# Performance work log

Measured on AMD Instinct MI355X. Metric: run time of the kernel, lower is better.

The kernel has to match this reference:

```python
import jax, jax.numpy as jnp
import numpy as np

B, T, F, H, C = 256, 14, 1024, 1024, 2513


def lstm_step(Wih, Whh, bih, bhh, x, h, c):
    # PyTorch LSTM cell: gate order i, f, g, o
    g = x @ Wih.T + bih + h @ Whh.T + bhh
    i, f, gg, o = jnp.split(g, 4, axis=-1)
    i = jax.nn.sigmoid(i)
    f = jax.nn.sigmoid(f)
    gg = jnp.tanh(gg)
    o = jax.nn.sigmoid(o)
    c = f * c + i * gg
    h = o * jnp.tanh(c)
    return h, c


def setup_inputs() -> dict:
    key = jax.random.key(0)
    ks = jax.random.split(key, 11)
    s = 1.0 / np.sqrt(H)
    u = lambda k, shape: jax.random.uniform(k, shape, jnp.float32, -s, s)
    return {
        "inputs": jax.random.normal(ks[0], (B, T, F), jnp.float32),
        "roll_Wih": u(ks[1], (4 * H, F)),
        "roll_Whh": u(ks[2], (4 * H, H)),
        "roll_bih": u(ks[3], (4 * H,)),
        "roll_bhh": u(ks[4], (4 * H,)),
        "unroll_Wih": u(ks[5], (4 * H, F)),
        "unroll_Whh": u(ks[6], (4 * H, H)),
        "unroll_bih": u(ks[7], (4 * H,)),
        "unroll_bhh": u(ks[8], (4 * H,)),
        "cls_W": u(ks[9], (C, H)),
        "cls_b": u(ks[10], (C,)),
    }


def reference(inputs, roll_Wih, roll_Whh, roll_bih, roll_bhh,
              unroll_Wih, unroll_Whh, unroll_bih, unroll_bhh, cls_W, cls_b):
    x_t = jnp.transpose(inputs, (1, 0, 2))  # [T, B, F]

    # Rolling LSTM: scan over time, keep hidden/cell at every step
    h0 = jnp.zeros((B, H), inputs.dtype)
    c0 = jnp.zeros((B, H), inputs.dtype)

    def roll(carry, xt):
        h, c = carry
        h, c = lstm_step(roll_Wih, roll_Whh, roll_bih, roll_bhh, xt, h, c)
        return (h, c), (h, c)

    _, (hs, cs) = jax.lax.scan(roll, (h0, c0), x_t)  # each [T, B, H]

    # Unrolling LSTM: for each t, feed inputs[t] repeated (T - t + 1) times,
    # starting from (hs[t], cs[t]). Vectorized over t: run T+1 steps for all
    # branches with constant per-branch input x_t[t], then pick step (T - t).
    def unroll(carry, _):
        h, c = carry  # [T, B, H]
        h, c = lstm_step(unroll_Wih, unroll_Whh, unroll_bih, unroll_bhh, x_t, h, c)
        return (h, c), h

    _, h_all = jax.lax.scan(unroll, (hs, cs), None, length=T + 1)  # [T+1, T, B, H]
    t_idx = jnp.arange(T)
    h_n = h_all[T - t_idx, t_idx]  # [T, B, H], last output of each branch

    x = jnp.transpose(h_n, (1, 0, 2))  # [B, T, H]
    y = x @ cls_W.T + cls_b  # [B, T, C]
    return y
```

## Files before the change

### kernel.cpp

```cpp
#include <hip/hip_runtime.h>

#define DEVFN __device__ __forceinline__

typedef __bf16 bf16x8 __attribute__((ext_vector_type(8)));
typedef float floatx4 __attribute__((ext_vector_type(4)));
typedef unsigned short us4 __attribute__((ext_vector_type(4)));


DEVFN unsigned short f2bf(float x) {
    union { float f; unsigned u; } v; v.f = x;
    v.u += 0x7FFFu + ((v.u >> 16) & 1u);
    return (unsigned short)(v.u >> 16);
}

DEVFN float bf2f(unsigned short s) {
    union { unsigned u; float f; } v; v.u = ((unsigned)s) << 16; return v.f;
}

DEVFN float sigm(float x) { return 1.f / (1.f + __expf(-x)); }
DEVFN float tanh_fast(float x) { float t = __expf(2.f * x); return 1.f - 2.f / (t + 1.f); }

DEVFN void gload_lds16(const unsigned short* g, unsigned short* l) {
    __builtin_amdgcn_global_load_lds(
        (__attribute__((address_space(1))) unsigned int*)g,
        (__attribute__((address_space(3))) unsigned int*)l, 16, 0, 0);
}

#define CFENCE asm volatile("" ::: "memory")


__global__ __launch_bounds__(256) void transpose_bt(const float* __restrict__ in,
                                                    unsigned short* __restrict__ out) {
    int idx = blockIdx.x * 256 + threadIdx.x;
    int k4 = (idx & 255) << 2;
    int row = idx >> 8;
    int t = row >> 8, b = row & 255;
    float4 v = *(const float4*)(in + (size_t)(b * 14 + t) * 1024 + k4);
    us4 o = {f2bf(v.x), f2bf(v.y), f2bf(v.z), f2bf(v.w)};
    *(us4*)(out + (size_t)row * 1024 + k4) = o;
}

__global__ __launch_bounds__(256) void conv_w4(const float* __restrict__ s0, const float* __restrict__ s1,
                                               const float* __restrict__ s2, const float* __restrict__ s3,
                                               unsigned short* __restrict__ d0, unsigned short* __restrict__ d1,
                                               unsigned short* __restrict__ d2, unsigned short* __restrict__ d3) {
    int t = blockIdx.x * 256 + threadIdx.x;
    int which = t >> 20;
    int off = (t & 1048575) << 2;
    const float* s = (which == 0) ? s0 : (which == 1) ? s1 : (which == 2) ? s2 : s3;
    unsigned short* d = (which == 0) ? d0 : (which == 1) ? d1 : (which == 2) ? d2 : d3;
    float4 v = *(const float4*)(s + off);
    us4 o = {f2bf(v.x), f2bf(v.y), f2bf(v.z), f2bf(v.w)};
    *(us4*)(d + off) = o;
}

__global__ __launch_bounds__(256) void conv_cls(const float* __restrict__ in,
                                                unsigned short* __restrict__ out) {
    int t = blockIdx.x * 256 + threadIdx.x;
    int off = t << 2;
    us4 o = {0, 0, 0, 0};
    if (off < 2573312) {
        float4 v = *(const float4*)(in + off);
        o = (us4){f2bf(v.x), f2bf(v.y), f2bf(v.z), f2bf(v.w)};
    }
    *(us4*)(out + off) = o;
}

__global__ __launch_bounds__(256) void bias_interleave(const float* __restrict__ a,
                                                       const float* __restrict__ b,
                                                       float* __restrict__ o4, int n) {
    int i = blockIdx.x * 256 + threadIdx.x;
    if (i < n) {
        int g = i >> 10, h = i & 1023;
        o4[h * 4 + g] = a[i] + b[i];
    }
}

__global__ __launch_bounds__(256) void cell_only(const unsigned short* __restrict__ pre4b,
                                                 float* __restrict__ c_out,
                                                 unsigned short* __restrict__ h_out) {
    int idx = blockIdx.x * 256 + threadIdx.x;
    us4 pv = *(const us4*)(pre4b + (size_t)idx * 4);
    float iv = sigm(bf2f(pv.x)), fv = sigm(bf2f(pv.y));
    float gv = tanh_fast(bf2f(pv.z)), ov = sigm(bf2f(pv.w));
    float cn = iv * gv;
    float hn = ov * tanh_fast(cn);
    c_out[idx] = cn;
    h_out[idx] = f2bf(hn);
}

template <int MODE, int NH>
__global__ __launch_bounds__(256, 2)
void lstm_big(const unsigned short* __restrict__ A1, const unsigned short* __restrict__ W1,
              const unsigned short* __restrict__ pre4b,
              const float* __restrict__ bias4,
              const float* __restrict__ c_in,
              float* __restrict__ c_out,
              unsigned short* __restrict__ h_out,
              unsigned short* __restrict__ h_alt, int retire_t,
              unsigned short* __restrict__ gout_bf,
              const float* __restrict__ clsb,
              float* __restrict__ outp, int gx) {
    constexpr int BROWS = 4 * NH;
    constexpr int FN = BROWS / 32;
    constexpr int BISS = BROWS / 64;
    constexpr int LOADS = 2 + BISS;
    constexpr int ASH = 4096;
    constexpr int BSH = BROWS * 32;
    constexpr int HH = NH / 32;

    __shared__ __align__(16) unsigned short lds[2][ASH + BSH];

    const int tid = threadIdx.x;
    const int nwg = gridDim.x;
    int id = blockIdx.x;
    id = ((id & 7) * (nwg >> 3)) + (id >> 3);
    const int bx = id % gx;
    const int by = id / gx;
    const int m0 = by * 128;
    const int n0h = bx * NH;
    const int n0c = bx * BROWS;
    const int lane = tid & 63;
    const int wv = tid >> 6;
    const int wm = wv >> 1, wn = wv & 1;
    const int r16 = lane & 15;
    const int kg = lane >> 4;

    auto stage = [&](int u, int buf) {
        const int ko = u * 32;
#pragma unroll
        for (int is = 0; is < 2; ++is) {
            int c = is * 256 + tid;
            int row = c >> 2, kq = c & 3;
            int kqg = kq ^ ((row >> 1) & 3);
            gload_lds16(A1 + (size_t)(m0 + row) * 1024 + ko + kqg * 8, &lds[buf][c * 8]);
        }
#pragma unroll
        for (int is = 0; is < BISS; ++is) {
            int c = is * 256 + tid;
            int row = c >> 2, kq = c & 3;
            int kqg = kq ^ ((row >> 1) & 3);
            int wr;
            if (MODE == 2) wr = n0c + row;
            else wr = ((row >> 4) & 3) * 1024 + n0h + ((row >> 6) << 4) + (row & 15);
            gload_lds16(W1 + (size_t)wr * 1024 + ko + kqg * 8, &lds[buf][ASH + c * 8]);
        }
    };

    floatx4 acc[4][FN];
#pragma unroll
    for (int i = 0; i < 4; ++i)
#pragma unroll
        for (int j = 0; j < FN; ++j) acc[i][j] = {0.f, 0.f, 0.f, 0.f};

    stage(0, 0);
    stage(1, 1);
    asm volatile("s_waitcnt vmcnt(%0)" :: "n"(LOADS) : "memory");
    __builtin_amdgcn_s_barrier();
    CFENCE;

#pragma unroll 2
    for (int u = 0; u < 32; ++u) {
        const int cur = u & 1;
        bf16x8 a[4], b[FN];
#pragma unroll
        for (int i = 0; i < 4; ++i) {
            int row = wm * 64 + i * 16 + r16;
            a[i] = *(const bf16x8*)&lds[cur][row * 32 + (kg ^ ((row >> 1) & 3)) * 8];
        }
#pragma unroll
        for (int j = 0; j < FN; ++j) {
            int row = wn * (BROWS / 2) + j * 16 + r16;
            b[j] = *(const bf16x8*)&lds[cur][ASH + row * 32 + (kg ^ ((row >> 1) & 3)) * 8];
        }
        __builtin_amdgcn_s_setprio(1);
#pragma unroll
        for (int i = 0; i < 4; ++i)
#pragma unroll
            for (int j = 0; j < FN; ++j)
                acc[i][j] = __builtin_amdgcn_mfma_f32_16x16x32_bf16(a[i], b[j], acc[i][j], 0, 0, 0);
        __builtin_amdgcn_s_setprio(0);

        if (u < 31) {
            __builtin_amdgcn_s_barrier();
            if (u < 30) {
                stage(u + 2, cur);
                asm volatile("s_waitcnt vmcnt(%0)" :: "n"(LOADS) : "memory");
            } else {
                asm volatile("s_waitcnt vmcnt(0)" ::: "memory");
            }
            __builtin_amdgcn_s_barrier();
            CFENCE;
        }
    }

    if (MODE == 2) {
#pragma unroll
        for (int i = 0; i < 4; ++i)
#pragma unroll
            for (int j = 0; j < FN; ++j)
#pragma unroll
                for (int rg = 0; rg < 4; ++rg) {
                    int m = m0 + wm * 64 + i * 16 + kg * 4 + rg;
                    int gn = n0c + wn * (BROWS / 2) + j * 16 + r16;
                    if (gn < 2513) {
                        int bb = m & 255, tt = m >> 8;
                        outp[(size_t)(bb * 14 + tt) * 2513 + gn] = acc[i][j][rg] + clsb[gn];
                    }
                }
        return;
    }

    unsigned short* hw = h_out;
    if (MODE == 1 && (m0 >> 8) == retire_t) hw = h_alt;

#pragma unroll
    for (int hh = 0; hh < HH; ++hh) {
        const int h = n0h + wn * (NH / 2) + hh * 16 + r16;
        float4 bv = make_float4(0.f, 0.f, 0.f, 0.f);
        if (MODE == 3 && bias4) bv = *(const float4*)(bias4 + (size_t)h * 4);
#pragma unroll
        for (int i = 0; i < 4; ++i)
#pragma unroll
            for (int rg = 0; rg < 4; ++rg) {
                int m = m0 + wm * 64 + i * 16 + kg * 4 + rg;
                size_t mh = (size_t)m * 1024 + h;
                float gi_ = acc[i][hh * 4 + 0][rg] + bv.x;
                float gf_ = acc[i][hh * 4 + 1][rg] + bv.y;
                float gg_ = acc[i][hh * 4 + 2][rg] + bv.z;
                float go_ = acc[i][hh * 4 + 3][rg] + bv.w;
                if (MODE == 3) {
                    us4 o = {f2bf(gi_), f2bf(gf_), f2bf(gg_), f2bf(go_)};
                    *(us4*)(gout_bf + mh * 4) = o;
                } else {
                    us4 pv = *(const us4*)(pre4b + mh * 4);
                    gi_ += bf2f(pv.x); gf_ += bf2f(pv.y);
                    gg_ += bf2f(pv.z); go_ += bf2f(pv.w);
                    float co = c_in[mh];
                    float iv = sigm(gi_), fv = sigm(gf_);
                    float gv = tanh_fast(gg_), ov = sigm(go_);
                    float cn = fv * co + iv * gv;
                    float hn = ov * tanh_fast(cn);
                    c_out[mh] = cn;
                    hw[mh] = f2bf(hn);
                }
            }
    }
}

__global__ __launch_bounds__(256)
void lstm_small(const unsigned short* __restrict__ A1, const unsigned short* __restrict__ W1,
                const unsigned short* __restrict__ pre4b,
                const float* __restrict__ c_in,
                float* __restrict__ c_out,
                unsigned short* __restrict__ h_out,
                unsigned short* __restrict__ h_alt, int retire_t,
                int gx) {
    constexpr int ATILE = 32 * 64;
    constexpr int LOADS = 5;

    __shared__ __align__(16) unsigned short lds[4][ATILE + 8192];

    const int tid = threadIdx.x;
    const int nwg = gridDim.x;
    int id = blockIdx.x;
    id = ((id & 7) * (nwg >> 3)) + (id >> 3);
    const int bx = id % gx;
    const int by = id / gx;
    const int m0 = by * 32;
    const int n0 = bx * 32;
    const int lane = tid & 63;
    const int wv = tid >> 6;
    const int wm = wv >> 1, wn = wv & 1;
    const int r16 = lane & 15;
    const int kg = lane >> 4;

    auto stage = [&](int kt, int buf) {
        const int ko = kt * 64;
        {
            int c = tid;
            int row = c >> 3, kq = c & 7, kqg = kq ^ (row & 7);
            gload_lds16(A1 + (size_t)(m0 + row) * 1024 + ko + kqg * 8, &lds[buf][c * 8]);
        }
#pragma unroll
        for (int is = 0; is < 4; ++is) {
            int c = is * 256 + tid;
            int row = c >> 3, kq = c & 7, kqg = kq ^ (row & 7);
            int wr = ((row >> 4) & 3) * 1024 + n0 + ((row >> 6) << 4) + (row & 15);
            gload_lds16(W1 + (size_t)wr * 1024 + ko + kqg * 8, &lds[buf][ATILE + c * 8]);
        }
    };

    floatx4 acc[4];
#pragma unroll
    for (int j = 0; j < 4; ++j) acc[j] = {0.f, 0.f, 0.f, 0.f};

    stage(0, 0);
    stage(1, 1);
    stage(2, 2);
    asm volatile("s_waitcnt vmcnt(%0)" :: "n"(2 * LOADS) : "memory");
    __builtin_amdgcn_s_barrier();
    CFENCE;

#pragma unroll 4
    for (int u = 0; u < 16; ++u) {
        const int cur = u & 3;
#pragma unroll
        for (int kk = 0; kk < 2; ++kk) {
            bf16x8 a, b[4];
            const int kqg = kk * 4 + kg;
            {
                int row = wm * 16 + r16;
                a = *(const bf16x8*)&lds[cur][row * 64 + (kqg ^ (row & 7)) * 8];
            }
#pragma unroll
            for (int j = 0; j < 4; ++j) {
                int row = wn * 64 + j * 16 + r16;
                b[j] = *(const bf16x8*)&lds[cur][ATILE + row * 64 + (kqg ^ (row & 7)) * 8];
            }
#pragma unroll
            for (int j = 0; j < 4; ++j)
                acc[j] = __builtin_amdgcn_mfma_f32_16x16x32_bf16(a, b[j], acc[j], 0, 0, 0);
        }
        if (u < 15) {
            __builtin_amdgcn_s_barrier();
            if (u < 13) {
                stage(u + 3, (u + 3) & 3);
                asm volatile("s_waitcnt vmcnt(%0)" :: "n"(2 * LOADS) : "memory");
            } else if (u == 13) {
                asm volatile("s_waitcnt vmcnt(%0)" :: "n"(LOADS) : "memory");
            } else {
                asm volatile("s_waitcnt vmcnt(0)" ::: "memory");
            }
            __builtin_amdgcn_s_barrier();
            CFENCE;
        }
    }

    const int h = n0 + wn * 16 + r16;
    unsigned short* hw = h_out;
    if ((m0 >> 8) == retire_t) hw = h_alt;

#pragma unroll
    for (int rg = 0; rg < 4; ++rg) {
        int m = m0 + wm * 16 + kg * 4 + rg;
        size_t mh = (size_t)m * 1024 + h;
        us4 pv = *(const us4*)(pre4b + mh * 4);
        float gi_ = acc[0][rg] + bf2f(pv.x);
        float gf_ = acc[1][rg] + bf2f(pv.y);
        float gg_ = acc[2][rg] + bf2f(pv.z);
        float go_ = acc[3][rg] + bf2f(pv.w);
        float co = c_in[mh];
        float iv = sigm(gi_), fv = sigm(gf_);
        float gv = tanh_fast(gg_), ov = sigm(go_);
        float cn = fv * co + iv * gv;
        float hn = ov * tanh_fast(cn);
        c_out[mh] = cn;
        hw[mh] = f2bf(hn);
    }
}


extern "C" void kernel_launch(void* const* d_in, const int* in_sizes, int n_in,
                              void* d_out, int out_size, void* d_ws, size_t ws_size,
                              hipStream_t stream) {
    (void)in_sizes; (void)n_in; (void)out_size; (void)ws_size;
    const float* inputs   = (const float*)d_in[0];
    const float* roll_Wih = (const float*)d_in[1];
    const float* roll_Whh = (const float*)d_in[2];
    const float* roll_bih = (const float*)d_in[3];
    const float* roll_bhh = (const float*)d_in[4];
    const float* un_Wih   = (const float*)d_in[5];
    const float* un_Whh   = (const float*)d_in[6];
    const float* un_bih   = (const float*)d_in[7];
    const float* un_bhh   = (const float*)d_in[8];
    const float* cls_Wf   = (const float*)d_in[9];
    const float* cls_b    = (const float*)d_in[10];
    float* out = (float*)d_out;

    char* ws = (char*)d_ws;
    size_t off = 0;
    auto alloc = [&](size_t bytes) -> char* {
        char* p = ws + off;
        off += (bytes + 255) & ~(size_t)255;
        return p;
    };
    unsigned short* xt   = (unsigned short*)alloc(3584ull * 1024 * 2);
    unsigned short* rWih = (unsigned short*)alloc(4096ull * 1024 * 2);
    unsigned short* rWhh = (unsigned short*)alloc(4096ull * 1024 * 2);
    unsigned short* uWih = (unsigned short*)alloc(4096ull * 1024 * 2);
    unsigned short* uWhh = (unsigned short*)alloc(4096ull * 1024 * 2);
    unsigned short* cWp  = (unsigned short*)alloc(2560ull * 1024 * 2);
    float* rbias4 = (float*)alloc(1024 * 4 * 4);
    float* ubias4 = (float*)alloc(1024 * 4 * 4);
    unsigned short* XpreB  = (unsigned short*)alloc(3584ull * 4096 * 2);
    unsigned short* XrollB = (unsigned short*)alloc(3584ull * 4096 * 2);
    float* uc     = (float*)alloc(3584ull * 1024 * 4);
    unsigned short* hb0    = (unsigned short*)alloc(3584ull * 1024 * 2);
    unsigned short* hb1    = (unsigned short*)alloc(3584ull * 1024 * 2);
    unsigned short* hfinal = (unsigned short*)alloc(3584ull * 1024 * 2);

    const size_t SF = 256 * 1024;

    transpose_bt<<<3584, 256, 0, stream>>>(inputs, xt);
    conv_w4<<<16384, 256, 0, stream>>>(roll_Wih, roll_Whh, un_Wih, un_Whh,
                                       rWih, rWhh, uWih, uWhh);
    conv_cls<<<2560, 256, 0, stream>>>(cls_Wf, cWp);
    bias_interleave<<<16, 256, 0, stream>>>(roll_bih, roll_bhh, rbias4, 4096);
    bias_interleave<<<16, 256, 0, stream>>>(un_bih, un_bhh, ubias4, 4096);

    lstm_big<3, 64><<<448, 256, 0, stream>>>(
        xt, uWih, nullptr, ubias4, nullptr, nullptr, nullptr, nullptr, -1,
        XpreB, nullptr, nullptr, 16);
    lstm_big<3, 64><<<448, 256, 0, stream>>>(
        xt, rWih, nullptr, rbias4, nullptr, nullptr, nullptr, nullptr, -1,
        XrollB, nullptr, nullptr, 16);

    cell_only<<<1024, 256, 0, stream>>>(XrollB, uc, hb0);
    for (int t = 1; t < 14; ++t) {
        lstm_small<<<256, 256, 0, stream>>>(
            hb0 + (size_t)(t - 1) * SF, rWhh,
            XrollB + (size_t)t * SF * 4,
            uc + (size_t)(t - 1) * SF, uc + (size_t)t * SF,
            hb0 + (size_t)t * SF, nullptr, -1, 32);
    }

    for (int s = 0; s <= 14; ++s) {
        int nb = (15 - s < 14) ? (15 - s) : 14;
        int M = nb * 256;
        const unsigned short* hsrc = (s & 1) ? hb1 : hb0;
        unsigned short* hdst = (s & 1) ? hb0 : hb1;
        int rt = (s >= 1) ? (14 - s) : -1;
        if (M >= 2304) {
            lstm_big<1, 64><<<M / 8, 256, 0, stream>>>(
                hsrc, uWhh, XpreB, nullptr, uc, uc, hdst, hfinal, rt,
                nullptr, nullptr, nullptr, 16);
        } else if (M >= 1024) {
            lstm_big<1, 32><<<M / 4, 256, 0, stream>>>(
                hsrc, uWhh, XpreB, nullptr, uc, uc, hdst, hfinal, rt,
                nullptr, nullptr, nullptr, 32);
        } else {
            lstm_small<<<M, 256, 0, stream>>>(
                hsrc, uWhh, XpreB, uc, uc, hdst, hfinal, rt, 32);
        }
    }

    lstm_big<2, 64><<<280, 256, 0, stream>>>(
        hfinal, cWp, nullptr, nullptr, nullptr, nullptr, nullptr, nullptr, -1,
        nullptr, cls_b, out, 10);
}
```

Baseline: 782.9 us.

## Merge input projections into one launch, fuse first cell step, use nontemporal stores

The two input-projection GEMMs (unroll and roll weights) are merged into a single 896-block launch (MODE 4). Each block picks its weight and bias set by column half. For the roll half at t=0, the first LSTM cell is computed directly in the epilogue, which removes the separate cell_only kernel and the round trip of those preactivations through memory. Block-to-tile mapping is replaced with fixed swizzles, and c/h/output accesses use nontemporal loads and stores to cut cache pollution. The changes add complexity, and the hardcoded swizzles assume the current grid sizes.

Result: slower. 832.7 us (+6.4%).

```diff
diff --git a/kernel.cpp b/kernel.cpp
--- a/kernel.cpp
+++ b/kernel.cpp
@@ -76,29 +76,20 @@
     }
 }
 
-__global__ __launch_bounds__(256) void cell_only(const unsigned short* __restrict__ pre4b,
-                                                 float* __restrict__ c_out,
-                                                 unsigned short* __restrict__ h_out) {
-    int idx = blockIdx.x * 256 + threadIdx.x;
-    us4 pv = *(const us4*)(pre4b + (size_t)idx * 4);
-    float iv = sigm(bf2f(pv.x)), fv = sigm(bf2f(pv.y));
-    float gv = tanh_fast(bf2f(pv.z)), ov = sigm(bf2f(pv.w));
-    float cn = iv * gv;
-    float hn = ov * tanh_fast(cn);
-    c_out[idx] = cn;
-    h_out[idx] = f2bf(hn);
-}
-
 template <int MODE, int NH>
 __global__ __launch_bounds__(256, 2)
-void lstm_big(const unsigned short* __restrict__ A1, const unsigned short* __restrict__ W1,
+void lstm_big(const unsigned short* __restrict__ A1,
+              const unsigned short* __restrict__ W1,
+              const unsigned short* __restrict__ W2,
               const unsigned short* __restrict__ pre4b,
-              const float* __restrict__ bias4,
+              const float* __restrict__ bias4a,
+              const float* __restrict__ bias4b,
               const float* __restrict__ c_in,
               float* __restrict__ c_out,
               unsigned short* __restrict__ h_out,
               unsigned short* __restrict__ h_alt, int retire_t,
-              unsigned short* __restrict__ gout_bf,
+              unsigned short* __restrict__ g1,
+              unsigned short* __restrict__ g2,
               const float* __restrict__ clsb,
               float* __restrict__ outp, int gx) {
     constexpr int BROWS = 4 * NH;
@@ -112,19 +103,31 @@
     __shared__ __align__(16) unsigned short lds[2][ASH + BSH];
 
     const int tid = threadIdx.x;
-    const int nwg = gridDim.x;
-    int id = blockIdx.x;
-    id = ((id & 7) * (nwg >> 3)) + (id >> 3);
-    const int bx = id % gx;
-    const int by = id / gx;
+    const int b = blockIdx.x;
+    int bx, by;
+    if (MODE == 2) {
+        int id = ((b & 7) * ((int)gridDim.x >> 3)) + (b >> 3);
+        bx = id % gx; by = id / gx;
+    } else if (MODE == 4) {
+        bx = ((b & 7) << 1) + ((b >> 3) & 1) + (((b >> 4) & 1) << 4);
+        by = b >> 5;
+    } else if (NH == 64) {
+        bx = ((b & 7) << 1) + ((b >> 3) & 1);
+        by = b >> 4;
+    } else {
+        bx = ((b & 7) << 2) + ((b >> 3) & 3);
+        by = b >> 5;
+    }
     const int m0 = by * 128;
-    const int n0h = bx * NH;
+    const int n0h = (MODE == 4) ? (bx & 15) * 64 : bx * NH;
     const int n0c = bx * BROWS;
     const int lane = tid & 63;
     const int wv = tid >> 6;
     const int wm = wv >> 1, wn = wv & 1;
     const int r16 = lane & 15;
     const int kg = lane >> 4;
+
+    const unsigned short* Ws = (MODE == 4 && (bx >> 4)) ? W2 : W1;
 
     auto stage = [&](int u, int buf) {
         const int ko = u * 32;
@@ -143,7 +146,7 @@
             int wr;
             if (MODE == 2) wr = n0c + row;
             else wr = ((row >> 4) & 3) * 1024 + n0h + ((row >> 6) << 4) + (row & 15);
-            gload_lds16(W1 + (size_t)wr * 1024 + ko + kqg * 8, &lds[buf][ASH + c * 8]);
+            gload_lds16(Ws + (size_t)wr * 1024 + ko + kqg * 8, &lds[buf][ASH + c * 8]);
         }
     };
 
@@ -162,7 +165,7 @@
 #pragma unroll 2
     for (int u = 0; u < 32; ++u) {
         const int cur = u & 1;
-        bf16x8 a[4], b[FN];
+        bf16x8 a[4], bfr[FN];
 #pragma unroll
         for (int i = 0; i < 4; ++i) {
             int row = wm * 64 + i * 16 + r16;
@@ -171,14 +174,14 @@
 #pragma unroll
         for (int j = 0; j < FN; ++j) {
             int row = wn * (BROWS / 2) + j * 16 + r16;
-            b[j] = *(const bf16x8*)&lds[cur][ASH + row * 32 + (kg ^ ((row >> 1) & 3)) * 8];
+            bfr[j] = *(const bf16x8*)&lds[cur][ASH + row * 32 + (kg ^ ((row >> 1) & 3)) * 8];
         }
         __builtin_amdgcn_s_setprio(1);
 #pragma unroll
         for (int i = 0; i < 4; ++i)
 #pragma unroll
             for (int j = 0; j < FN; ++j)
-                acc[i][j] = __builtin_amdgcn_mfma_f32_16x16x32_bf16(a[i], b[j], acc[i][j], 0, 0, 0);
+                acc[i][j] = __builtin_amdgcn_mfma_f32_16x16x32_bf16(a[i], bfr[j], acc[i][j], 0, 0, 0);
         __builtin_amdgcn_s_setprio(0);
 
         if (u < 31) {
@@ -205,45 +208,72 @@
                     int gn = n0c + wn * (BROWS / 2) + j * 16 + r16;
                     if (gn < 2513) {
                         int bb = m & 255, tt = m >> 8;
-                        outp[(size_t)(bb * 14 + tt) * 2513 + gn] = acc[i][j][rg] + clsb[gn];
+                        __builtin_nontemporal_store(acc[i][j][rg] + clsb[gn],
+                                                    outp + (size_t)(bb * 14 + tt) * 2513 + gn);
                     }
                 }
         return;
     }
 
+    if (MODE == 4) {
+        const int half = bx >> 4;
+        unsigned short* gsel = half ? g2 : g1;
+        const float* bsel = half ? bias4b : bias4a;
+        const bool cell0 = (half == 1) && (by < 2);
+#pragma unroll
+        for (int hh = 0; hh < HH; ++hh) {
+            const int h = n0h + wn * (NH / 2) + hh * 16 + r16;
+            float4 bv = *(const float4*)(bsel + (size_t)h * 4);
+#pragma unroll
+            for (int i = 0; i < 4; ++i)
+#pragma unroll
+                for (int rg = 0; rg < 4; ++rg) {
+                    int m = m0 + wm * 64 + i * 16 + kg * 4 + rg;
+                    size_t mh = (size_t)m * 1024 + h;
+                    float gi_ = acc[i][hh * 4 + 0][rg] + bv.x;
+                    float gf_ = acc[i][hh * 4 + 1][rg] + bv.y;
+                    float gg_ = acc[i][hh * 4 + 2][rg] + bv.z;
+                    float go_ = acc[i][hh * 4 + 3][rg] + bv.w;
+                    if (cell0) {
+                        float iv = sigm(gi_), ov = sigm(go_);
+                        float gv = tanh_fast(gg_);
+                        float cn = iv * gv;
+                        float hn = ov * tanh_fast(cn);
+                        __builtin_nontemporal_store(cn, c_out + mh);
+                        __builtin_nontemporal_store(f2bf(hn), h_out + mh);
+                    } else {
+                        us4 o = {f2bf(gi_), f2bf(gf_), f2bf(gg_), f2bf(go_)};
+                        __builtin_nontemporal_store(o, (us4*)(gsel + mh * 4));
+                    }
+                }
+        }
+        return;
+    }
+
     unsigned short* hw = h_out;
-    if (MODE == 1 && (m0 >> 8) == retire_t) hw = h_alt;
+    if ((m0 >> 8) == retire_t) hw = h_alt;
 
 #pragma unroll
     for (int hh = 0; hh < HH; ++hh) {
         const int h = n0h + wn * (NH / 2) + hh * 16 + r16;
-        float4 bv = make_float4(0.f, 0.f, 0.f, 0.f);
-        if (MODE == 3 && bias4) bv = *(const float4*)(bias4 + (size_t)h * 4);
 #pragma unroll
         for (int i = 0; i < 4; ++i)
 #pragma unroll
             for (int rg = 0; rg < 4; ++rg) {
                 int m = m0 + wm * 64 + i * 16 + kg * 4 + rg;
                 size_t mh = (size_t)m * 1024 + h;
-                float gi_ = acc[i][hh * 4 + 0][rg] + bv.x;
-                float gf_ = acc[i][hh * 4 + 1][rg] + bv.y;
-                float gg_ = acc[i][hh * 4 + 2][rg] + bv.z;
-                float go_ = acc[i][hh * 4 + 3][rg] + bv.w;
-                if (MODE == 3) {
-                    us4 o = {f2bf(gi_), f2bf(gf_), f2bf(gg_), f2bf(go_)};
-                    *(us4*)(gout_bf + mh * 4) = o;
-                } else {
-                    us4 pv = *(const us4*)(pre4b + mh * 4);
-                    gi_ += bf2f(pv.x); gf_ += bf2f(pv.y);
-                    gg_ += bf2f(pv.z); go_ += bf2f(pv.w);
-                    float co = c_in[mh];
-                    float iv = sigm(gi_), fv = sigm(gf_);
-                    float gv = tanh_fast(gg_), ov = sigm(go_);
-                    float cn = fv * co + iv * gv;
-                    float hn = ov * tanh_fast(cn);
-                    c_out[mh] = cn;
-                    hw[mh] = f2bf(hn);
-                }
+                us4 pv = *(const us4*)(pre4b + mh * 4);
+                float gi_ = acc[i][hh * 4 + 0][rg] + bf2f(pv.x);
+                float gf_ = acc[i][hh * 4 + 1][rg] + bf2f(pv.y);
+                float gg_ = acc[i][hh * 4 + 2][rg] + bf2f(pv.z);
+                float go_ = acc[i][hh * 4 + 3][rg] + bf2f(pv.w);
+                float co = __builtin_nontemporal_load(c_in + mh);
+                float iv = sigm(gi_), fv = sigm(gf_);
+                float gv = tanh_fast(gg_), ov = sigm(go_);
+                float cn = fv * co + iv * gv;
+                float hn = ov * tanh_fast(cn);
+                __builtin_nontemporal_store(cn, c_out + mh);
+                __builtin_nontemporal_store(f2bf(hn), hw + mh);
             }
     }
 }
@@ -254,19 +284,16 @@
                 const float* __restrict__ c_in,
                 float* __restrict__ c_out,
                 unsigned short* __restrict__ h_out,
-                unsigned short* __restrict__ h_alt, int retire_t,
-                int gx) {
+                unsigned short* __restrict__ h_alt, int retire_t) {
     constexpr int ATILE = 32 * 64;
     constexpr int LOADS = 5;
 
     __shared__ __align__(16) unsigned short lds[4][ATILE + 8192];
 
     const int tid = threadIdx.x;
-    const int nwg = gridDim.x;
-    int id = blockIdx.x;
-    id = ((id & 7) * (nwg >> 3)) + (id >> 3);
-    const int bx = id % gx;
-    const int by = id / gx;
+    const int b = blockIdx.x;
+    const int bx = ((b & 7) << 2) + ((b >> 3) & 3);
+    const int by = b >> 5;
     const int m0 = by * 32;
     const int n0 = bx * 32;
     const int lane = tid & 63;
@@ -307,7 +334,7 @@
         const int cur = u & 3;
 #pragma unroll
         for (int kk = 0; kk < 2; ++kk) {
-            bf16x8 a, b[4];
+            bf16x8 a, bfr[4];
             const int kqg = kk * 4 + kg;
             {
                 int row = wm * 16 + r16;
@@ -316,11 +343,11 @@
 #pragma unroll
             for (int j = 0; j < 4; ++j) {
                 int row = wn * 64 + j * 16 + r16;
-                b[j] = *(const bf16x8*)&lds[cur][ATILE + row * 64 + (kqg ^ (row & 7)) * 8];
+                bfr[j] = *(const bf16x8*)&lds[cur][ATILE + row * 64 + (kqg ^ (row & 7)) * 8];
             }
 #pragma unroll
             for (int j = 0; j < 4; ++j)
-                acc[j] = __builtin_amdgcn_mfma_f32_16x16x32_bf16(a, b[j], acc[j], 0, 0, 0);
+                acc[j] = __builtin_amdgcn_mfma_f32_16x16x32_bf16(a, bfr[j], acc[j], 0, 0, 0);
         }
         if (u < 15) {
             __builtin_amdgcn_s_barrier();
@@ -350,13 +377,13 @@
         float gf_ = acc[1][rg] + bf2f(pv.y);
         float gg_ = acc[2][rg] + bf2f(pv.z);
         float go_ = acc[3][rg] + bf2f(pv.w);
-        float co = c_in[mh];
+        float co = __builtin_nontemporal_load(c_in + mh);
         float iv = sigm(gi_), fv = sigm(gf_);
         float gv = tanh_fast(gg_), ov = sigm(go_);
         float cn = fv * co + iv * gv;
         float hn = ov * tanh_fast(cn);
-        c_out[mh] = cn;
-        hw[mh] = f2bf(hn);
+        __builtin_nontemporal_store(cn, c_out + mh);
+        __builtin_nontemporal_store(f2bf(hn), hw + mh);
     }
 }
 
@@ -409,20 +436,16 @@
     bias_interleave<<<16, 256, 0, stream>>>(roll_bih, roll_bhh, rbias4, 4096);
     bias_interleave<<<16, 256, 0, stream>>>(un_bih, un_bhh, ubias4, 4096);
 
-    lstm_big<3, 64><<<448, 256, 0, stream>>>(
-        xt, uWih, nullptr, ubias4, nullptr, nullptr, nullptr, nullptr, -1,
-        XpreB, nullptr, nullptr, 16);
-    lstm_big<3, 64><<<448, 256, 0, stream>>>(
-        xt, rWih, nullptr, rbias4, nullptr, nullptr, nullptr, nullptr, -1,
-        XrollB, nullptr, nullptr, 16);
-
-    cell_only<<<1024, 256, 0, stream>>>(XrollB, uc, hb0);
+    lstm_big<4, 64><<<896, 256, 0, stream>>>(
+        xt, uWih, rWih, nullptr, ubias4, rbias4,
+        nullptr, uc, hb0, nullptr, -1, XpreB, XrollB, nullptr, nullptr, 32);
+
     for (int t = 1; t < 14; ++t) {
         lstm_small<<<256, 256, 0, stream>>>(
             hb0 + (size_t)(t - 1) * SF, rWhh,
             XrollB + (size_t)t * SF * 4,
             uc + (size_t)(t - 1) * SF, uc + (size_t)t * SF,
-            hb0 + (size_t)t * SF, nullptr, -1, 32);
+            hb0 + (size_t)t * SF, nullptr, -1);
     }
 
     for (int s = 0; s <= 14; ++s) {
@@ -433,19 +456,19 @@
         int rt = (s >= 1) ? (14 - s) : -1;
         if (M >= 2304) {
             lstm_big<1, 64><<<M / 8, 256, 0, stream>>>(
-                hsrc, uWhh, XpreB, nullptr, uc, uc, hdst, hfinal, rt,
-                nullptr, nullptr, nullptr, 16);
+                hsrc, uWhh, nullptr, XpreB, nullptr, nullptr,
+                uc, uc, hdst, hfinal, rt, nullptr, nullptr, nullptr, nullptr, 16);
         } else if (M >= 1024) {
             lstm_big<1, 32><<<M / 4, 256, 0, stream>>>(
-                hsrc, uWhh, XpreB, nullptr, uc, uc, hdst, hfinal, rt,
-                nullptr, nullptr, nullptr, 32);
+                hsrc, uWhh, nullptr, XpreB, nullptr, nullptr,
+                uc, uc, hdst, hfinal, rt, nullptr, nullptr, nullptr, nullptr, 32);
         } else {
             lstm_small<<<M, 256, 0, stream>>>(
-                hsrc, uWhh, XpreB, uc, uc, hdst, hfinal, rt, 32);
+                hsrc, uWhh, XpreB, uc, uc, hdst, hfinal, rt);
         }
     }
 
     lstm_big<2, 64><<<280, 256, 0, stream>>>(
-        hfinal, cWp, nullptr, nullptr, nullptr, nullptr, nullptr, nullptr, -1,
-        nullptr, cls_b, out, 10);
-}
+        hfinal, cWp, nullptr, nullptr, nullptr, nullptr,
+        nullptr, nullptr, nullptr, nullptr, -1, nullptr, nullptr, cls_b, out, 10);
+}
```
